# Kernel tuning notes

Hardware: AMD Instinct MI355X
Metric: run time of the kernel (lower is better)

## Reference

```python
import math
import jax, jax.numpy as jnp
import numpy as np

B_, L_, D_, N_, R_ = 4, 1024, 1024, 16, 64  # batch, seq, n_embd(=dim_inner), d_state, dt_rank


def setup_inputs() -> dict:
    key = jax.random.key(0)
    ks = jax.random.split(key, 6)
    s = lambda k, shp: jax.random.normal(k, shp, jnp.float32) * 0.02
    return {
        "x": jax.random.normal(ks[0], (B_, L_, D_), jnp.float32),
        "ln1_w": jnp.ones((D_,), jnp.float32),
        "ln2_w": jnp.ones((D_,), jnp.float32),
        "W_dbc": s(ks[1], (R_ + 2 * N_, D_)),   # x -> [delta_lowrank, B, C]
        "W_dt": s(ks[2], (D_, R_)),              # dt_rank -> dim_inner
        "b_dt": jnp.zeros((D_,), jnp.float32),
        "A_log": jnp.log(jnp.broadcast_to(jnp.arange(1, N_ + 1, dtype=jnp.float32), (D_, N_))),
        "Dp": jnp.ones((D_,), jnp.float32),      # skip-connection D parameter
        "W_fc": s(ks[3], (4 * D_, D_)),
        "W_proj": s(ks[4], (D_, 4 * D_)),
    }


def _layernorm(x, w):
    mu = jnp.mean(x, -1, keepdims=True)
    xc = x - mu
    var = jnp.mean(xc * xc, -1, keepdims=True)
    return xc * jax.lax.rsqrt(var + 1e-5) * w


def _new_gelu(x):
    c = math.sqrt(2.0 / math.pi)
    return 0.5 * x * (1.0 + jnp.tanh(c * (x + 0.044715 * x * x * x)))


def _ssm(x, W_dbc, W_dt, b_dt, A_log, Dp):
    # x: (b, l, d) with d == dim_inner == n_embd
    dbc = jnp.einsum("bld,ed->ble", x, W_dbc)                # (b,l,R+2N)
    delta, Bm, Cm = jnp.split(dbc, [R_, R_ + N_], axis=-1)
    delta = jax.nn.softplus(jnp.einsum("blr,dr->bld", delta, W_dt) + b_dt)  # (b,l,d)
    A = -jnp.exp(A_log)                                       # (d,n)
    dA = jnp.exp(delta[..., None] * A)                        # (b,l,d,n) discretized A
    dBx = (delta * x)[..., None] * Bm[:, :, None, :]          # (b,l,d,n) discretized B*x

    # h_t = dA_t * h_{t-1} + dBx_t  -> parallel first-order linear scan
    def combine(e1, e2):
        a1, b1 = e1
        a2, b2 = e2
        return a2 * a1, a2 * b1 + b2

    _, hs = jax.lax.associative_scan(combine, (dA, dBx), axis=1)
    y = jnp.einsum("bldn,bln->bld", hs, Cm)
    return y + x * Dp


def reference(x, ln1_w, ln2_w, W_dbc, W_dt, b_dt, A_log, Dp, W_fc, W_proj):
    h = jax.nn.softplus(_layernorm(x, ln1_w))
    h = h + _ssm(h, W_dbc, W_dt, b_dt, A_log, Dp)
    m = _layernorm(h, ln2_w)
    m = _new_gelu(jnp.einsum("bld,fd->blf", m, W_fc))
    m = jnp.einsum("blf,df->bld", m, W_proj)
    return h + m
```

## Files before the change

kernel.cpp:

```cpp
#include <hip/hip_runtime.h>
#include <cstdint>
#include <cstddef>

typedef unsigned short u16;
typedef unsigned int u32;
typedef __attribute__((ext_vector_type(8))) short short8;
typedef __attribute__((ext_vector_type(4))) float floatx4;
typedef __attribute__((ext_vector_type(4))) u16 u16x4;

#define DEV static __device__ __forceinline__

DEV u16 f2b(float f){ u32 u = __float_as_uint(f); u32 r = u + 0x7fffu + ((u>>16)&1u); return (u16)(r>>16); }
DEV float softplusf(float z){ return fmaxf(z,0.f) + log1pf(__expf(-fabsf(z))); }
DEV float fast_tanhf(float u){ float e = __expf(2.f*u); return 1.f - 2.f/(e+1.f); }
DEV float geluf(float x){ float u = 0.7978845608028654f*(x + 0.044715f*x*x*x); return 0.5f*x*(1.f+fast_tanhf(u)); }

DEV void async_copy16(const void* gp, void* lp){
  __builtin_amdgcn_global_load_lds((const __attribute__((address_space(1))) u32*)gp,
                                   (__attribute__((address_space(3))) u32*)lp, 16, 0, 0);
}

__global__ __launch_bounds__(256)
void prep_weights(const float* __restrict__ Wdbc, const float* __restrict__ Wdt,
                  const float* __restrict__ Wfc, const float* __restrict__ Wproj,
                  u16* __restrict__ dbc_b, u16* __restrict__ dt_b,
                  u16* __restrict__ fc_b, u16* __restrict__ pj_b)
{
  int i = blockIdx.x*256 + threadIdx.x;
  const float* src; u16* dst; int j;
  if (i < 32768){
    int e = i*4, r = e >> 10;
    if (r >= 96){ u16x4 z = {0,0,0,0}; *(u16x4*)(dbc_b + e) = z; return; }
    src = Wdbc; dst = dbc_b; j = i;
  } else if (i < 49152){ src = Wdt;   dst = dt_b; j = i - 32768; }
  else if (i < 1097728){ src = Wfc;   dst = fc_b; j = i - 49152; }
  else                 { src = Wproj; dst = pj_b; j = i - 1097728; }
  float4 v = ((const float4*)src)[j];
  u16x4 o = { f2b(v.x), f2b(v.y), f2b(v.z), f2b(v.w) };
  *(u16x4*)(dst + j*4) = o;
}

__global__ void dbc_post(const float* __restrict__ p, u16* __restrict__ delta_in,
                         float* __restrict__ BCf){
  int e = blockIdx.x*256 + threadIdx.x;
  int t = e >> 7, c = e & 127;
  float s = 0.f;
  #pragma unroll
  for (int z=0;z<8;z++) s += p[(size_t)z*524288 + e];
  if (c < 64)      delta_in[t*64 + c] = f2b(s);
  else if (c < 96) BCf[t*32 + (c-64)] = s;
}

__global__ void proj_reduce(const float* __restrict__ p, const float* __restrict__ h1f,
                            float* __restrict__ out){
  int i = blockIdx.x*256 + threadIdx.x;
  float4 a = ((const float4*)p)[i];
  float4 b = ((const float4*)(p + (size_t)4194304))[i];
  float4 r = ((const float4*)h1f)[i];
  float4 o = make_float4(a.x+b.x+r.x, a.y+b.y+r.y, a.z+b.z+r.z, a.w+b.w+r.w);
  ((float4*)out)[i] = o;
}

__global__ __launch_bounds__(256)
void ln1_kernel(const float* __restrict__ x, const float* __restrict__ w,
                float* __restrict__ h0f, u16* __restrict__ h0b)
{
  int row = blockIdx.x, tid = threadIdx.x;
  const float4* xr = (const float4*)(x + (size_t)row*1024);
  float4 v = xr[tid];
  float s1 = v.x+v.y+v.z+v.w;
  float s2 = v.x*v.x+v.y*v.y+v.z*v.z+v.w*v.w;
  #pragma unroll
  for (int m=1;m<64;m<<=1){ s1 += __shfl_xor(s1,m); s2 += __shfl_xor(s2,m); }
  __shared__ float red[8];
  int wv = tid>>6;
  if ((tid&63)==0){ red[wv]=s1; red[4+wv]=s2; }
  __syncthreads();
  s1 = red[0]+red[1]+red[2]+red[3];
  s2 = red[4]+red[5]+red[6]+red[7];
  float mu  = s1*(1.f/1024.f);
  float var = s2*(1.f/1024.f) - mu*mu;
  float rstd = rsqrtf(var + 1e-5f);
  float4 wv4 = ((const float4*)w)[tid];
  float o0 = softplusf((v.x-mu)*rstd*wv4.x);
  float o1 = softplusf((v.y-mu)*rstd*wv4.y);
  float o2 = softplusf((v.z-mu)*rstd*wv4.z);
  float o3 = softplusf((v.w-mu)*rstd*wv4.w);
  ((float4*)(h0f + (size_t)row*1024))[tid] = make_float4(o0,o1,o2,o3);
  u16x4 ob = { f2b(o0), f2b(o1), f2b(o2), f2b(o3) };
  *(u16x4*)(h0b + (size_t)row*1024 + tid*4) = ob;
}

__global__ __launch_bounds__(256)
void ln2_kernel(const float* __restrict__ x, const float* __restrict__ w,
                u16* __restrict__ outb)
{
  int row = blockIdx.x, tid = threadIdx.x;
  const float4* xr = (const float4*)(x + (size_t)row*1024);
  float4 v = xr[tid];
  float s1 = v.x+v.y+v.z+v.w;
  float s2 = v.x*v.x+v.y*v.y+v.z*v.z+v.w*v.w;
  #pragma unroll
  for (int m=1;m<64;m<<=1){ s1 += __shfl_xor(s1,m); s2 += __shfl_xor(s2,m); }
  __shared__ float red[8];
  int wv = tid>>6;
  if ((tid&63)==0){ red[wv]=s1; red[4+wv]=s2; }
  __syncthreads();
  s1 = red[0]+red[1]+red[2]+red[3];
  s2 = red[4]+red[5]+red[6]+red[7];
  float mu  = s1*(1.f/1024.f);
  float var = s2*(1.f/1024.f) - mu*mu;
  float rstd = rsqrtf(var + 1e-5f);
  float4 wv4 = ((const float4*)w)[tid];
  u16x4 ob = { f2b((v.x-mu)*rstd*wv4.x), f2b((v.y-mu)*rstd*wv4.y),
               f2b((v.z-mu)*rstd*wv4.z), f2b((v.w-mu)*rstd*wv4.w) };
  *(u16x4*)(outb + (size_t)row*1024 + tid*4) = ob;
}

template<int EPI, int SWZ>
__global__ __launch_bounds__(256)
void gemm_bt(const u16* __restrict__ A, int lda,
             const u16* __restrict__ B, int ldb, int K,
             float* __restrict__ outF, u16* __restrict__ outB, int ldo,
             const float* __restrict__ bias, size_t zstr)
{
  __shared__ u16 sA[128*32];
  __shared__ u16 sB[128*32];
  const int tid = threadIdx.x;
  int m_blk, n_blk, zb;
  if (SWZ == 0){ n_blk = blockIdx.x; m_blk = blockIdx.y; zb = blockIdx.z; }
  else if (SWZ == 1){
    int b = blockIdx.x, xcd = b & 7, local = b >> 3;
    m_blk = (xcd>>2)*16 + (local & 15);
    n_blk = (xcd&3)*8 + (local >> 4);
    zb = 0;
  } else {
    int b = blockIdx.x, xcd = b & 7, local = b >> 3;
    m_blk = (xcd>>1)*8 + (local & 7);
    n_blk = local >> 3;
    zb = xcd & 1;
  }
  const int m0 = m_blk*128, n0 = n_blk*128;
  const int kstart = zb * K;
  const int wave = tid>>6, lane = tid&63;
  const int wm = (wave>>1)*64, wn = (wave&1)*64;
  const int lr = lane&15, quad = lane>>4;

  floatx4 acc[4][4];
  #pragma unroll
  for (int i=0;i<4;i++)
    #pragma unroll
    for (int j=0;j<4;j++){ floatx4 z = {0.f,0.f,0.f,0.f}; acc[i][j]=z; }

  const int r0 = tid>>2;
  const int kc8 = (((tid&3) ^ ((tid>>3)&3)))*8;
  const int sswz = ((lr>>1)&3);
  for (int k0=kstart; k0<kstart+K; k0+=32){
    __syncthreads();
    async_copy16(A + (size_t)(m0+r0)*lda    + k0+kc8, &sA[(size_t)tid*8]);
    async_copy16(A + (size_t)(m0+64+r0)*lda + k0+kc8, &sA[(size_t)(tid+256)*8]);
    async_copy16(B + (size_t)(n0+r0)*ldb    + k0+kc8, &sB[(size_t)tid*8]);
    async_copy16(B + (size_t)(n0+64+r0)*ldb + k0+kc8, &sB[(size_t)(tid+256)*8]);
    __syncthreads();
    short8 af[4], bf[4];
    #pragma unroll
    for (int i=0;i<4;i++){
      af[i] = *(const short8*)&sA[(wm+i*16+lr)*32 + (quad^sswz)*8];
      bf[i] = *(const short8*)&sB[(wn+i*16+lr)*32 + (quad^sswz)*8];
    }
    #pragma unroll
    for (int i=0;i<4;i++)
      #pragma unroll
      for (int j=0;j<4;j++)
        acc[i][j] = __builtin_amdgcn_mfma_f32_16x16x32_bf16(af[i], bf[j], acc[i][j], 0,0,0);
  }
  #pragma unroll
  for (int i=0;i<4;i++){
    #pragma unroll
    for (int j=0;j<4;j++){
      #pragma unroll
      for (int r=0;r<4;r++){
        int gr = m0 + wm + i*16 + quad*4 + r;
        int gc = n0 + wn + j*16 + lr;
        float v = acc[i][j][r];
        size_t o = (size_t)gr*ldo + gc;
        if (EPI==1)      outF[o] = softplusf(v + bias[gc]);
        else if (EPI==2) outB[o] = f2b(geluf(v));
        else             outF[zstr*zb + o] = v;
      }
    }
  }
}

__global__ __launch_bounds__(256)
void scan_p1(const float* __restrict__ delta, const float* __restrict__ h0f,
             const float* __restrict__ BCf, const float* __restrict__ A_log,
             float* __restrict__ Pbuf, float* __restrict__ Sbuf)
{
  int blk = blockIdx.x;
  int d = (blk & 3)*256 + threadIdx.x;
  int c = (blk >> 2) & 31;
  int b = blk >> 7;
  float a2[16], h[16], P[16];
  #pragma unroll
  for (int n=0;n<16;n++){ a2[n] = -__expf(A_log[d*16+n]) * 1.44269504f; h[n]=0.f; P[n]=1.f; }
  int t0 = c*32;
  const float* dptr = delta + ((size_t)(b*1024 + t0))*1024 + d;
  const float* xptr = h0f   + ((size_t)(b*1024 + t0))*1024 + d;
  const float* bc   = BCf   + ((size_t)(b*1024 + t0))*32;
  #pragma unroll 4
  for (int t=0;t<32;t++){
    float dlt = dptr[t*1024];
    float xv  = xptr[t*1024];
    float dx = dlt*xv;
    #pragma unroll
    for (int n=0;n<16;n++){
      float dA = exp2f(dlt*a2[n]);
      h[n] = dA*h[n] + dx*bc[t*32+n];
      P[n] *= dA;
    }
  }
  size_t base = ((size_t)((b*32 + c)*16))*1024 + d;
  #pragma unroll
  for (int n=0;n<16;n++){ Pbuf[base + (size_t)n*1024] = P[n]; Sbuf[base + (size_t)n*1024] = h[n]; }
}

__global__ __launch_bounds__(256)
void scan_p2(const float* __restrict__ Pbuf, const float* __restrict__ Sbuf,
             float* __restrict__ Hbuf)
{
  int blk = blockIdx.x;
  int d = (blk & 3)*256 + threadIdx.x;
  int n = (blk >> 2) & 15;
  int b = blk >> 6;
  float H = 0.f;
  for (int c=0;c<32;c++){
    size_t idx = ((size_t)((b*32 + c)*16 + n))*1024 + d;
    float P = Pbuf[idx], S = Sbuf[idx];
    Hbuf[idx] = H;
    H = P*H + S;
  }
}

__global__ __launch_bounds__(256)
void scan_p3(const float* __restrict__ delta, const float* __restrict__ h0f,
             const float* __restrict__ BCf, const float* __restrict__ A_log,
             const float* __restrict__ Hbuf, const float* __restrict__ Dp,
             float* __restrict__ h1f)
{
  int blk = blockIdx.x;
  int d = (blk & 3)*256 + threadIdx.x;
  int c = (blk >> 2) & 31;
  int b = blk >> 7;
  float a2[16], h[16];
  size_t hb = ((size_t)((b*32 + c)*16))*1024 + d;
  #pragma unroll
  for (int n=0;n<16;n++){
    a2[n] = -__expf(A_log[d*16+n]) * 1.44269504f;
    h[n] = Hbuf[hb + (size_t)n*1024];
  }
  float dpv = 1.f + Dp[d];
  int t0 = c*32;
  const float* dptr = delta + ((size_t)(b*1024 + t0))*1024 + d;
  const float* xptr = h0f   + ((size_t)(b*1024 + t0))*1024 + d;
  const float* bc   = BCf   + ((size_t)(b*1024 + t0))*32;
  float* optr = h1f + ((size_t)(b*1024 + t0))*1024 + d;
  #pragma unroll 4
  for (int t=0;t<32;t++){
    float dlt = dptr[t*1024];
    float xv  = xptr[t*1024];
    float dx = dlt*xv;
    float y = 0.f;
    #pragma unroll
    for (int n=0;n<16;n++){
      float dA = exp2f(dlt*a2[n]);
      h[n] = dA*h[n] + dx*bc[t*32+n];
      y += h[n]*bc[t*32+16+n];
    }
    optr[t*1024] = xv*dpv + y;
  }
}

extern "C" void kernel_launch(void* const* d_in, const int* in_sizes, int n_in,
                              void* d_out, int out_size, void* d_ws, size_t ws_size,
                              hipStream_t stream)
{
  const float* x    = (const float*)d_in[0];
  const float* ln1w = (const float*)d_in[1];
  const float* ln2w = (const float*)d_in[2];
  const float* Wdbc = (const float*)d_in[3];
  const float* Wdt  = (const float*)d_in[4];
  const float* bdt  = (const float*)d_in[5];
  const float* Alog = (const float*)d_in[6];
  const float* Dp   = (const float*)d_in[7];
  const float* Wfc  = (const float*)d_in[8];
  const float* Wproj= (const float*)d_in[9];
  float* out = (float*)d_out;

  char* ws = (char*)d_ws;
  size_t off = 0;
  auto carve = [&](size_t bytes)->char*{ char* p = ws + off; off += (bytes + 255) & ~(size_t)255; return p; };
  const size_t T = 4096;
  float* h0f   = (float*)carve(T*1024*4);
  float* h1f   = (float*)carve(T*1024*4);
  float* dlt   = (float*)carve(T*1024*4);
  float* Pbuf  = (float*)carve((size_t)4*32*16*1024*4);
  float* Sbuf  = (float*)carve((size_t)4*32*16*1024*4);
  float* Hbuf  = (float*)carve((size_t)4*32*16*1024*4);
  float* pad_  = (float*)carve((size_t)4*32*16*1024*4);
  float* BCf   = (float*)carve(T*32*4);
  u16*   h0b   = (u16*)  carve(T*1024*2);
  u16*   m0b   = (u16*)  carve(T*1024*2);
  u16*   g_b   = (u16*)  carve(T*4096*2);
  u16*   din_b = (u16*)  carve(T*64*2);
  u16*   Wdbc_b= (u16*)  carve((size_t)128*1024*2);
  u16*   Wdt_b = (u16*)  carve((size_t)1024*64*2);
  u16*   Wfc_b = (u16*)  carve((size_t)4096*1024*2);
  u16*   Wpj_b = (u16*)  carve((size_t)1024*4096*2);
  float* dbc_p  = Hbuf;
  float* proj_p = Pbuf;
  (void)pad_; (void)ws_size; (void)in_sizes; (void)n_in; (void)out_size;

  prep_weights<<<8384, 256, 0, stream>>>(Wdbc, Wdt, Wfc, Wproj,
                                         Wdbc_b, Wdt_b, Wfc_b, Wpj_b);

  ln1_kernel<<<4096, 256, 0, stream>>>(x, ln1w, h0f, h0b);

  gemm_bt<4,0><<<dim3(1,32,8), 256, 0, stream>>>(h0b, 1024, Wdbc_b, 1024, 128,
                                                 dbc_p, nullptr, 128, nullptr, (size_t)T*128);
  dbc_post<<<2048, 256, 0, stream>>>(dbc_p, din_b, BCf);

  gemm_bt<1,0><<<dim3(8,32), 256, 0, stream>>>(din_b, 64, Wdt_b, 64, 64,
                                               dlt, nullptr, 1024, bdt, 0);

  scan_p1<<<512, 256, 0, stream>>>(dlt, h0f, BCf, Alog, Pbuf, Sbuf);
  scan_p2<<<256, 256, 0, stream>>>(Pbuf, Sbuf, Hbuf);
  scan_p3<<<512, 256, 0, stream>>>(dlt, h0f, BCf, Alog, Hbuf, Dp, h1f);

  ln2_kernel<<<4096, 256, 0, stream>>>(h1f, ln2w, m0b);

  gemm_bt<2,1><<<1024, 256, 0, stream>>>(m0b, 1024, Wfc_b, 1024, 1024,
                                         nullptr, g_b, 4096, nullptr, 0);

  gemm_bt<4,2><<<512, 256, 0, stream>>>(g_b, 4096, Wpj_b, 4096, 2048,
                                        proj_p, nullptr, 1024, nullptr, (size_t)T*1024);
  proj_reduce<<<4096, 256, 0, stream>>>(proj_p, h1f, out);
}
```

Baseline: 356.7 us.

## Use 2-wave wide-tile GEMM for MLP and fuse split-K reduce via counters

Adds a gemm_wide kernel for the two big MLP GEMMs. It keeps the 128x128 tile but uses 2 waves of 128 threads, each computing a 128x64 slab with 8x4 MFMA accumulators, so fragment reuse per LDS read goes up at the cost of more registers. The split-K projection GEMM no longer needs a separate proj_reduce kernel: an atomic counter per output tile lets the last-finishing K-half add both partials plus the residual and write the output. This removes one launch and one full read and write pass, but adds fences, atomics and a memset, and lowers waves per block.

```diff
diff --git a/kernel.cpp b/kernel.cpp
--- a/kernel.cpp
+++ b/kernel.cpp
@@ -49,16 +49,6 @@
   for (int z=0;z<8;z++) s += p[(size_t)z*524288 + e];
   if (c < 64)      delta_in[t*64 + c] = f2b(s);
   else if (c < 96) BCf[t*32 + (c-64)] = s;
-}
-
-__global__ void proj_reduce(const float* __restrict__ p, const float* __restrict__ h1f,
-                            float* __restrict__ out){
-  int i = blockIdx.x*256 + threadIdx.x;
-  float4 a = ((const float4*)p)[i];
-  float4 b = ((const float4*)(p + (size_t)4194304))[i];
-  float4 r = ((const float4*)h1f)[i];
-  float4 o = make_float4(a.x+b.x+r.x, a.y+b.y+r.y, a.z+b.z+r.z, a.w+b.w+r.w);
-  ((float4*)out)[i] = o;
 }
 
 __global__ __launch_bounds__(256)
@@ -117,31 +107,18 @@
   *(u16x4*)(outb + (size_t)row*1024 + tid*4) = ob;
 }
 
-template<int EPI, int SWZ>
+template<int EPI>
 __global__ __launch_bounds__(256)
 void gemm_bt(const u16* __restrict__ A, int lda,
              const u16* __restrict__ B, int ldb, int K,
-             float* __restrict__ outF, u16* __restrict__ outB, int ldo,
+             float* __restrict__ outF, int ldo,
              const float* __restrict__ bias, size_t zstr)
 {
   __shared__ u16 sA[128*32];
   __shared__ u16 sB[128*32];
   const int tid = threadIdx.x;
-  int m_blk, n_blk, zb;
-  if (SWZ == 0){ n_blk = blockIdx.x; m_blk = blockIdx.y; zb = blockIdx.z; }
-  else if (SWZ == 1){
-    int b = blockIdx.x, xcd = b & 7, local = b >> 3;
-    m_blk = (xcd>>2)*16 + (local & 15);
-    n_blk = (xcd&3)*8 + (local >> 4);
-    zb = 0;
-  } else {
-    int b = blockIdx.x, xcd = b & 7, local = b >> 3;
-    m_blk = (xcd>>1)*8 + (local & 7);
-    n_blk = local >> 3;
-    zb = xcd & 1;
-  }
-  const int m0 = m_blk*128, n0 = n_blk*128;
-  const int kstart = zb * K;
+  const int m0 = blockIdx.y*128, n0 = blockIdx.x*128;
+  const int kstart = blockIdx.z * K;
   const int wave = tid>>6, lane = tid&63;
   const int wm = (wave>>1)*64, wn = (wave&1)*64;
   const int lr = lane&15, quad = lane>>4;
@@ -184,9 +161,106 @@
         int gc = n0 + wn + j*16 + lr;
         float v = acc[i][j][r];
         size_t o = (size_t)gr*ldo + gc;
-        if (EPI==1)      outF[o] = softplusf(v + bias[gc]);
-        else if (EPI==2) outB[o] = f2b(geluf(v));
-        else             outF[zstr*zb + o] = v;
+        if (EPI==1) outF[o] = softplusf(v + bias[gc]);
+        else        outF[zstr*blockIdx.z + o] = v;
+      }
+    }
+  }
+}
+
+template<int EPI, int SWZ>
+__global__ __launch_bounds__(128, 2)
+void gemm_wide(const u16* __restrict__ A, int lda,
+               const u16* __restrict__ B, int ldb, int K,
+               float* __restrict__ outF, u16* __restrict__ outB, int ldo,
+               size_t zstr, const float* __restrict__ h1f, int* __restrict__ counters)
+{
+  __shared__ u16 sA[128*32];
+  __shared__ u16 sB[128*32];
+  const int tid = threadIdx.x;
+  int m_blk, n_blk, zb;
+  if (SWZ == 1){
+    int b = blockIdx.x, xcd = b & 7, local = b >> 3;
+    m_blk = (xcd>>1)*8 + (local & 7);
+    n_blk = (xcd&1)*16 + (local >> 3);
+    zb = 0;
+  } else {
+    int b = blockIdx.x, xcd = b & 7, local = b >> 3;
+    m_blk = (xcd>>1)*8 + (local & 7);
+    n_blk = local >> 3;
+    zb = xcd & 1;
+  }
+  const int m0 = m_blk*128, n0 = n_blk*128;
+  const int kstart = zb * K;
+  const int lane = tid&63, wave = tid>>6;
+  const int wn = wave*64;
+  const int lr = lane&15, quad = lane>>4;
+
+  floatx4 acc[8][4];
+  #pragma unroll
+  for (int i=0;i<8;i++)
+    #pragma unroll
+    for (int j=0;j<4;j++){ floatx4 z = {0.f,0.f,0.f,0.f}; acc[i][j]=z; }
+
+  const int r0 = tid>>2;
+  const int kc8 = (((tid&3) ^ ((tid>>3)&3)))*8;
+  const int sswz = ((lr>>1)&3);
+  for (int k0=kstart; k0<kstart+K; k0+=32){
+    __syncthreads();
+    #pragma unroll
+    for (int p=0;p<4;p++){
+      async_copy16(A + (size_t)(m0+r0+32*p)*lda + k0+kc8, &sA[(size_t)tid*8 + p*1024]);
+      async_copy16(B + (size_t)(n0+r0+32*p)*ldb + k0+kc8, &sB[(size_t)tid*8 + p*1024]);
+    }
+    __syncthreads();
+    short8 af[8], bf[4];
+    #pragma unroll
+    for (int i=0;i<8;i++) af[i] = *(const short8*)&sA[(i*16+lr)*32 + (quad^sswz)*8];
+    #pragma unroll
+    for (int j=0;j<4;j++) bf[j] = *(const short8*)&sB[(wn+j*16+lr)*32 + (quad^sswz)*8];
+    #pragma unroll
+    for (int i=0;i<8;i++)
+      #pragma unroll
+      for (int j=0;j<4;j++)
+        acc[i][j] = __builtin_amdgcn_mfma_f32_16x16x32_bf16(af[i], bf[j], acc[i][j], 0,0,0);
+  }
+  #pragma unroll
+  for (int i=0;i<8;i++){
+    #pragma unroll
+    for (int j=0;j<4;j++){
+      #pragma unroll
+      for (int r=0;r<4;r++){
+        int gr = m0 + i*16 + quad*4 + r;
+        int gc = n0 + wn + j*16 + lr;
+        float v = acc[i][j][r];
+        size_t o = (size_t)gr*ldo + gc;
+        if (EPI==2) outB[o] = f2b(geluf(v));
+        else        outF[zstr*zb + o] = v;
+      }
+    }
+  }
+  if (EPI==5){
+    __shared__ int lastflag;
+    __threadfence();
+    __syncthreads();
+    if (tid==0){
+      int old = atomicAdd(&counters[m_blk*8 + n_blk], 1);
+      lastflag = (old==1);
+    }
+    __syncthreads();
+    if (lastflag){
+      __threadfence();
+      float* outP = (float*)outB;
+      #pragma unroll 4
+      for (int s=0;s<32;s++){
+        int q = s*128 + tid;
+        int r = q>>5, c4 = q&31;
+        size_t o = (size_t)(m0+r)*ldo + n0 + c4*4;
+        float4 a = *(const float4*)(outF + o);
+        float4 b = *(const float4*)(outF + zstr + o);
+        float4 h = *(const float4*)(h1f + o);
+        float4 res = make_float4(a.x+b.x+h.x, a.y+b.y+h.y, a.z+b.z+h.z, a.w+b.w+h.w);
+        *(float4*)(outP + o) = res;
       }
     }
   }
@@ -317,21 +391,24 @@
   u16*   Wdt_b = (u16*)  carve((size_t)1024*64*2);
   u16*   Wfc_b = (u16*)  carve((size_t)4096*1024*2);
   u16*   Wpj_b = (u16*)  carve((size_t)1024*4096*2);
+  int*   cnt   = (int*)  carve(256*4);
   float* dbc_p  = Hbuf;
   float* proj_p = Pbuf;
   (void)pad_; (void)ws_size; (void)in_sizes; (void)n_in; (void)out_size;
 
+  hipMemsetAsync(cnt, 0, 256*4, stream);
+
   prep_weights<<<8384, 256, 0, stream>>>(Wdbc, Wdt, Wfc, Wproj,
                                          Wdbc_b, Wdt_b, Wfc_b, Wpj_b);
 
   ln1_kernel<<<4096, 256, 0, stream>>>(x, ln1w, h0f, h0b);
 
-  gemm_bt<4,0><<<dim3(1,32,8), 256, 0, stream>>>(h0b, 1024, Wdbc_b, 1024, 128,
-                                                 dbc_p, nullptr, 128, nullptr, (size_t)T*128);
+  gemm_bt<4><<<dim3(1,32,8), 256, 0, stream>>>(h0b, 1024, Wdbc_b, 1024, 128,
+                                               dbc_p, 128, nullptr, (size_t)T*128);
   dbc_post<<<2048, 256, 0, stream>>>(dbc_p, din_b, BCf);
 
-  gemm_bt<1,0><<<dim3(8,32), 256, 0, stream>>>(din_b, 64, Wdt_b, 64, 64,
-                                               dlt, nullptr, 1024, bdt, 0);
+  gemm_bt<1><<<dim3(8,32), 256, 0, stream>>>(din_b, 64, Wdt_b, 64, 64,
+                                             dlt, 1024, bdt, 0);
 
   scan_p1<<<512, 256, 0, stream>>>(dlt, h0f, BCf, Alog, Pbuf, Sbuf);
   scan_p2<<<256, 256, 0, stream>>>(Pbuf, Sbuf, Hbuf);
@@ -339,10 +416,9 @@
 
   ln2_kernel<<<4096, 256, 0, stream>>>(h1f, ln2w, m0b);
 
-  gemm_bt<2,1><<<1024, 256, 0, stream>>>(m0b, 1024, Wfc_b, 1024, 1024,
-                                         nullptr, g_b, 4096, nullptr, 0);
-
-  gemm_bt<4,2><<<512, 256, 0, stream>>>(g_b, 4096, Wpj_b, 4096, 2048,
-                                        proj_p, nullptr, 1024, nullptr, (size_t)T*1024);
-  proj_reduce<<<4096, 256, 0, stream>>>(proj_p, h1f, out);
-}
+  gemm_wide<2,1><<<1024, 128, 0, stream>>>(m0b, 1024, Wfc_b, 1024, 1024,
+                                           nullptr, g_b, 4096, 0, nullptr, nullptr);
+
+  gemm_wide<5,2><<<512, 128, 0, stream>>>(g_b, 4096, Wpj_b, 4096, 2048,
+                                          proj_p, (u16*)out, 1024, (size_t)T*1024, h1f, cnt);
+}
```

Result: slower. 412.2 us (+15.5%).

## Fuse proj split-K reduction into GEMM via counters, read bf16 activations in scan

Applied to the files above, without the earlier changes.

The projection GEMM now uses 4-way split-K over 1024 blocks. The last-arriving block of each output tile, found with a per-tile atomic counter and thread fences, sums the partials plus the residual and writes the output directly, which removes the separate proj_reduce kernel. The fp32 copy of the LN1 output is dropped, so the scan kernels read the bf16 copy instead, cutting a 16MB write and two reads at the cost of some precision in the scan input and skip term. The dbc GEMM split-K factor drops from 8 to 4, so there are fewer partials to reduce. The workspace is re-laid out so the 64MB of proj partials fit, and a memset is added to zero the counters.

```diff
diff --git a/kernel.cpp b/kernel.cpp
--- a/kernel.cpp
+++ b/kernel.cpp
@@ -11,6 +11,7 @@
 #define DEV static __device__ __forceinline__
 
 DEV u16 f2b(float f){ u32 u = __float_as_uint(f); u32 r = u + 0x7fffu + ((u>>16)&1u); return (u16)(r>>16); }
+DEV float b2f(u16 u){ return __uint_as_float(((u32)u)<<16); }
 DEV float softplusf(float z){ return fmaxf(z,0.f) + log1pf(__expf(-fabsf(z))); }
 DEV float fast_tanhf(float u){ float e = __expf(2.f*u); return 1.f - 2.f/(e+1.f); }
 DEV float geluf(float x){ float u = 0.7978845608028654f*(x + 0.044715f*x*x*x); return 0.5f*x*(1.f+fast_tanhf(u)); }
@@ -46,24 +47,14 @@
   int t = e >> 7, c = e & 127;
   float s = 0.f;
   #pragma unroll
-  for (int z=0;z<8;z++) s += p[(size_t)z*524288 + e];
+  for (int z=0;z<4;z++) s += p[(size_t)z*524288 + e];
   if (c < 64)      delta_in[t*64 + c] = f2b(s);
   else if (c < 96) BCf[t*32 + (c-64)] = s;
 }
 
-__global__ void proj_reduce(const float* __restrict__ p, const float* __restrict__ h1f,
-                            float* __restrict__ out){
-  int i = blockIdx.x*256 + threadIdx.x;
-  float4 a = ((const float4*)p)[i];
-  float4 b = ((const float4*)(p + (size_t)4194304))[i];
-  float4 r = ((const float4*)h1f)[i];
-  float4 o = make_float4(a.x+b.x+r.x, a.y+b.y+r.y, a.z+b.z+r.z, a.w+b.w+r.w);
-  ((float4*)out)[i] = o;
-}
-
 __global__ __launch_bounds__(256)
 void ln1_kernel(const float* __restrict__ x, const float* __restrict__ w,
-                float* __restrict__ h0f, u16* __restrict__ h0b)
+                u16* __restrict__ h0b)
 {
   int row = blockIdx.x, tid = threadIdx.x;
   const float4* xr = (const float4*)(x + (size_t)row*1024);
@@ -86,7 +77,6 @@
   float o1 = softplusf((v.y-mu)*rstd*wv4.y);
   float o2 = softplusf((v.z-mu)*rstd*wv4.z);
   float o3 = softplusf((v.w-mu)*rstd*wv4.w);
-  ((float4*)(h0f + (size_t)row*1024))[tid] = make_float4(o0,o1,o2,o3);
   u16x4 ob = { f2b(o0), f2b(o1), f2b(o2), f2b(o3) };
   *(u16x4*)(h0b + (size_t)row*1024 + tid*4) = ob;
 }
@@ -122,7 +112,8 @@
 void gemm_bt(const u16* __restrict__ A, int lda,
              const u16* __restrict__ B, int ldb, int K,
              float* __restrict__ outF, u16* __restrict__ outB, int ldo,
-             const float* __restrict__ bias, size_t zstr)
+             const float* __restrict__ bias, size_t zstr,
+             const float* __restrict__ h1f, int* __restrict__ counters)
 {
   __shared__ u16 sA[128*32];
   __shared__ u16 sB[128*32];
@@ -136,9 +127,9 @@
     zb = 0;
   } else {
     int b = blockIdx.x, xcd = b & 7, local = b >> 3;
-    m_blk = (xcd>>1)*8 + (local & 7);
-    n_blk = local >> 3;
-    zb = xcd & 1;
+    zb = xcd >> 1;
+    n_blk = (xcd&1)*4 + (local & 3);
+    m_blk = local >> 2;
   }
   const int m0 = m_blk*128, n0 = n_blk*128;
   const int kstart = zb * K;
@@ -190,10 +181,38 @@
       }
     }
   }
-}
-
-__global__ __launch_bounds__(256)
-void scan_p1(const float* __restrict__ delta, const float* __restrict__ h0f,
+  if (EPI==5){
+    __shared__ int lastflag;
+    __threadfence();
+    __syncthreads();
+    if (tid==0){
+      int old = atomicAdd(&counters[m_blk*8 + n_blk], 1);
+      lastflag = (old==3);
+    }
+    __syncthreads();
+    if (lastflag){
+      __threadfence();
+      float* outP = (float*)outB;
+      #pragma unroll 4
+      for (int s=0;s<16;s++){
+        int q = s*256 + tid;
+        int r = q>>5, c4 = q&31;
+        size_t o = (size_t)(m0+r)*ldo + n0 + c4*4;
+        float4 a0 = *(const float4*)(outF + o);
+        float4 a1 = *(const float4*)(outF + zstr + o);
+        float4 a2 = *(const float4*)(outF + 2*zstr + o);
+        float4 a3 = *(const float4*)(outF + 3*zstr + o);
+        float4 h  = *(const float4*)(h1f + o);
+        float4 res = make_float4(a0.x+a1.x+a2.x+a3.x+h.x, a0.y+a1.y+a2.y+a3.y+h.y,
+                                 a0.z+a1.z+a2.z+a3.z+h.z, a0.w+a1.w+a2.w+a3.w+h.w);
+        *(float4*)(outP + o) = res;
+      }
+    }
+  }
+}
+
+__global__ __launch_bounds__(256)
+void scan_p1(const float* __restrict__ delta, const u16* __restrict__ h0b,
              const float* __restrict__ BCf, const float* __restrict__ A_log,
              float* __restrict__ Pbuf, float* __restrict__ Sbuf)
 {
@@ -206,16 +225,16 @@
   for (int n=0;n<16;n++){ a2[n] = -__expf(A_log[d*16+n]) * 1.44269504f; h[n]=0.f; P[n]=1.f; }
   int t0 = c*32;
   const float* dptr = delta + ((size_t)(b*1024 + t0))*1024 + d;
-  const float* xptr = h0f   + ((size_t)(b*1024 + t0))*1024 + d;
+  const u16*   xptr = h0b   + ((size_t)(b*1024 + t0))*1024 + d;
   const float* bc   = BCf   + ((size_t)(b*1024 + t0))*32;
   #pragma unroll 4
   for (int t=0;t<32;t++){
-    float dlt = dptr[t*1024];
-    float xv  = xptr[t*1024];
-    float dx = dlt*xv;
+    float dlv = dptr[t*1024];
+    float xv  = b2f(xptr[t*1024]);
+    float dx = dlv*xv;
     #pragma unroll
     for (int n=0;n<16;n++){
-      float dA = exp2f(dlt*a2[n]);
+      float dA = exp2f(dlv*a2[n]);
       h[n] = dA*h[n] + dx*bc[t*32+n];
       P[n] *= dA;
     }
@@ -243,7 +262,7 @@
 }
 
 __global__ __launch_bounds__(256)
-void scan_p3(const float* __restrict__ delta, const float* __restrict__ h0f,
+void scan_p3(const float* __restrict__ delta, const u16* __restrict__ h0b,
              const float* __restrict__ BCf, const float* __restrict__ A_log,
              const float* __restrict__ Hbuf, const float* __restrict__ Dp,
              float* __restrict__ h1f)
@@ -262,18 +281,18 @@
   float dpv = 1.f + Dp[d];
   int t0 = c*32;
   const float* dptr = delta + ((size_t)(b*1024 + t0))*1024 + d;
-  const float* xptr = h0f   + ((size_t)(b*1024 + t0))*1024 + d;
+  const u16*   xptr = h0b   + ((size_t)(b*1024 + t0))*1024 + d;
   const float* bc   = BCf   + ((size_t)(b*1024 + t0))*32;
   float* optr = h1f + ((size_t)(b*1024 + t0))*1024 + d;
   #pragma unroll 4
   for (int t=0;t<32;t++){
-    float dlt = dptr[t*1024];
-    float xv  = xptr[t*1024];
-    float dx = dlt*xv;
+    float dlv = dptr[t*1024];
+    float xv  = b2f(xptr[t*1024]);
+    float dx = dlv*xv;
     float y = 0.f;
     #pragma unroll
     for (int n=0;n<16;n++){
-      float dA = exp2f(dlt*a2[n]);
+      float dA = exp2f(dlv*a2[n]);
       h[n] = dA*h[n] + dx*bc[t*32+n];
       y += h[n]*bc[t*32+16+n];
     }
@@ -301,48 +320,53 @@
   size_t off = 0;
   auto carve = [&](size_t bytes)->char*{ char* p = ws + off; off += (bytes + 255) & ~(size_t)255; return p; };
   const size_t T = 4096;
-  float* h0f   = (float*)carve(T*1024*4);
-  float* h1f   = (float*)carve(T*1024*4);
-  float* dlt   = (float*)carve(T*1024*4);
-  float* Pbuf  = (float*)carve((size_t)4*32*16*1024*4);
-  float* Sbuf  = (float*)carve((size_t)4*32*16*1024*4);
-  float* Hbuf  = (float*)carve((size_t)4*32*16*1024*4);
-  float* pad_  = (float*)carve((size_t)4*32*16*1024*4);
-  float* BCf   = (float*)carve(T*32*4);
-  u16*   h0b   = (u16*)  carve(T*1024*2);
-  u16*   m0b   = (u16*)  carve(T*1024*2);
-  u16*   g_b   = (u16*)  carve(T*4096*2);
-  u16*   din_b = (u16*)  carve(T*64*2);
-  u16*   Wdbc_b= (u16*)  carve((size_t)128*1024*2);
-  u16*   Wdt_b = (u16*)  carve((size_t)1024*64*2);
-  u16*   Wfc_b = (u16*)  carve((size_t)4096*1024*2);
-  u16*   Wpj_b = (u16*)  carve((size_t)1024*4096*2);
+  float* h1f     = (float*)carve(T*1024*4);
+  float* delta_f = (float*)carve(T*1024*4);
+  float* Pbuf    = (float*)carve((size_t)4*32*16*1024*4);
+  float* Sbuf    = (float*)carve((size_t)4*32*16*1024*4);
+  float* Hbuf    = (float*)carve((size_t)4*32*16*1024*4);
+  float* padx    = (float*)carve((size_t)24*1024*1024);
+  float* BCf = (float*)carve(T*32*4);
+  u16* h0b = (u16*)carve(T*1024*2);
+  u16* m0b = (u16*)carve(T*1024*2);
+  u16* g_b = (u16*)carve(T*4096*2);
+  u16* din_b = (u16*)carve(T*64*2);
+  u16* Wdbc_b = (u16*)carve((size_t)128*1024*2);
+  u16* Wdt_b = (u16*)carve((size_t)1024*64*2);
+  u16* Wfc_b = (u16*)carve((size_t)4096*1024*2);
+  u16* Wpj_b = (u16*)carve((size_t)1024*4096*2);
+  int* cnt = (int*)carve(256*4);
   float* dbc_p  = Hbuf;
-  float* proj_p = Pbuf;
-  (void)pad_; (void)ws_size; (void)in_sizes; (void)n_in; (void)out_size;
+  float* proj_p = delta_f;
+  (void)padx; (void)ws_size; (void)in_sizes; (void)n_in; (void)out_size;
+
+  (void)hipMemsetAsync(cnt, 0, 256*4, stream);
 
   prep_weights<<<8384, 256, 0, stream>>>(Wdbc, Wdt, Wfc, Wproj,
                                          Wdbc_b, Wdt_b, Wfc_b, Wpj_b);
 
-  ln1_kernel<<<4096, 256, 0, stream>>>(x, ln1w, h0f, h0b);
-
-  gemm_bt<4,0><<<dim3(1,32,8), 256, 0, stream>>>(h0b, 1024, Wdbc_b, 1024, 128,
-                                                 dbc_p, nullptr, 128, nullptr, (size_t)T*128);
+  ln1_kernel<<<4096, 256, 0, stream>>>(x, ln1w, h0b);
+
+  gemm_bt<4,0><<<dim3(1,32,4), 256, 0, stream>>>(h0b, 1024, Wdbc_b, 1024, 256,
+                                                 dbc_p, nullptr, 128, nullptr, (size_t)T*128,
+                                                 nullptr, nullptr);
   dbc_post<<<2048, 256, 0, stream>>>(dbc_p, din_b, BCf);
 
   gemm_bt<1,0><<<dim3(8,32), 256, 0, stream>>>(din_b, 64, Wdt_b, 64, 64,
-                                               dlt, nullptr, 1024, bdt, 0);
-
-  scan_p1<<<512, 256, 0, stream>>>(dlt, h0f, BCf, Alog, Pbuf, Sbuf);
+                                               delta_f, nullptr, 1024, bdt, 0,
+                                               nullptr, nullptr);
+
+  scan_p1<<<512, 256, 0, stream>>>(delta_f, h0b, BCf, Alog, Pbuf, Sbuf);
   scan_p2<<<256, 256, 0, stream>>>(Pbuf, Sbuf, Hbuf);
-  scan_p3<<<512, 256, 0, stream>>>(dlt, h0f, BCf, Alog, Hbuf, Dp, h1f);
+  scan_p3<<<512, 256, 0, stream>>>(delta_f, h0b, BCf, Alog, Hbuf, Dp, h1f);
 
   ln2_kernel<<<4096, 256, 0, stream>>>(h1f, ln2w, m0b);
 
   gemm_bt<2,1><<<1024, 256, 0, stream>>>(m0b, 1024, Wfc_b, 1024, 1024,
-                                         nullptr, g_b, 4096, nullptr, 0);
-
-  gemm_bt<4,2><<<512, 256, 0, stream>>>(g_b, 4096, Wpj_b, 4096, 2048,
-                                        proj_p, nullptr, 1024, nullptr, (size_t)T*1024);
-  proj_reduce<<<4096, 256, 0, stream>>>(proj_p, h1f, out);
-}
+                                         nullptr, g_b, 4096, nullptr, 0,
+                                         nullptr, nullptr);
+
+  gemm_bt<5,2><<<1024, 256, 0, stream>>>(g_b, 4096, Wpj_b, 4096, 1024,
+                                         proj_p, (u16*)out, 1024, nullptr, (size_t)T*1024,
+                                         h1f, cnt);
+}
```

Result: slower. 613.7 us (+72.0%).
